# Kernel optimization log

Hardware: AMD Instinct MI355X
Metric: run time of the kernel (lower is better)

Reference implementation:

```python
import jax, jax.numpy as jnp
import numpy as np

N_HEAD = 16
BLOCK = 128  # segment length sl=128, dilation ratio dr=1 (hardcoded in forward)


def setup_inputs() -> dict:
    key = jax.random.key(0)
    k1, k2, k3 = jax.random.split(key, 3)
    B, T, C = 4, 8192, 2048
    x = jax.random.normal(k1, (B, T, C), dtype=jnp.float32)
    W_qkv = jax.random.normal(k2, (C, 3 * C), dtype=jnp.float32) * 0.02
    W_proj = jax.random.normal(k3, (C, C), dtype=jnp.float32) * 0.02
    return {"x": x, "W_qkv": W_qkv, "W_proj": W_proj}


def reference(x, W_qkv, W_proj):
    B, T, C = x.shape
    H = N_HEAD
    dh = C // H
    nb = T // BLOCK  # number of 128-token segments

    qkv = x @ W_qkv                      # (B, T, 3C)
    q, k, v = jnp.split(qkv, 3, axis=-1)

    def to_blocks(t):
        # (B, T, C) -> (B, nb, H, BLOCK, dh)
        return t.reshape(B, nb, BLOCK, H, dh).transpose(0, 1, 3, 2, 4)

    q, k, v = to_blocks(q), to_blocks(k), to_blocks(v)

    scale = 1.0 / jnp.sqrt(jnp.asarray(dh, dtype=x.dtype))
    scores = jnp.einsum('bnhqd,bnhkd->bnhqk', q, k) * scale  # (B, nb, H, BLOCK, BLOCK)
    causal = jnp.tril(jnp.ones((BLOCK, BLOCK), dtype=bool))
    scores = jnp.where(causal, scores, -jnp.inf)
    att = jax.nn.softmax(scores, axis=-1)
    out = jnp.einsum('bnhqk,bnhkd->bnhqd', att, v)
    # Single (sl, dr) branch => lse-weighted scattering collapses to weight 1.
    y = out.transpose(0, 1, 3, 2, 4).reshape(B, T, C)
    return y @ W_proj
```

## Files before the change

### kernel.cpp

```cpp
#include <hip/hip_runtime.h>

typedef unsigned short u16;
typedef unsigned int u32;
typedef __bf16 bf16x8 __attribute__((ext_vector_type(8)));
typedef float f32x4 __attribute__((ext_vector_type(4)));

#define DIM_M 32768
#define DIM_C 2048
#define DIM_3C 6144
#define N_HEAD 16
#define DH 128

__device__ __forceinline__ u16 f2bf(float f) {
  u32 x = __float_as_uint(f);
  u32 r = x + 0x7fffu + ((x >> 16) & 1u);
  return (u16)(r >> 16);
}

__device__ __forceinline__ void async_copy16(const void* g, void* l) {
  __builtin_amdgcn_global_load_lds((const __attribute__((address_space(1))) u32*)g,
                                   (__attribute__((address_space(3))) u32*)l,
                                   16, 0, 0);
}

__device__ __forceinline__ void phase_bar() {
  asm volatile("" ::: "memory");
  __builtin_amdgcn_sched_barrier(0);
  __builtin_amdgcn_s_barrier();
  __builtin_amdgcn_sched_barrier(0);
  asm volatile("" ::: "memory");
}

__global__ __launch_bounds__(256) void cvt_f32_bf16(const float* __restrict__ in,
                                                    u16* __restrict__ out) {
  size_t i = ((size_t)blockIdx.x * 256 + threadIdx.x) * 4;
  float4 v = *(const float4*)(in + i);
  union { u16 s[4]; uint2 u; } o;
  o.s[0] = f2bf(v.x); o.s[1] = f2bf(v.y); o.s[2] = f2bf(v.z); o.s[3] = f2bf(v.w);
  *(uint2*)(out + i) = o.u;
}

__global__ __launch_bounds__(256) void transpose_cvt(const float* __restrict__ W,
                                                     u16* __restrict__ Wt,
                                                     int K, int N) {
  __shared__ u16 t[32][33];
  int nb = blockIdx.x * 32, kb = blockIdx.y * 32;
  int r = threadIdx.x >> 5, c = threadIdx.x & 31;
#pragma unroll
  for (int i = 0; i < 4; ++i) {
    int rr = i * 8 + r;
    t[rr][c] = f2bf(W[(size_t)(kb + rr) * N + nb + c]);
  }
  __syncthreads();
#pragma unroll
  for (int i = 0; i < 4; ++i) {
    int rr = i * 8 + r;
    Wt[(size_t)(nb + rr) * K + kb + c] = t[c][rr];
  }
}

#define STAGE(OP, BUF, KOFF)                                                        \
  do {                                                                              \
    _Pragma("unroll") for (int l_ = 0; l_ < 4; ++l_)                                \
        async_copy16(g##OP + (size_t)l_ * 64 * K + (KOFF),                          \
                     &s##OP[BUF][(l_ * 8 + w) * 512]);                              \
  } while (0)

#define LDA_Q(QA)                                                                   \
  do {                                                                              \
    _Pragma("unroll") for (int f_ = 0; f_ < 4; ++f_)                                \
        _Pragma("unroll") for (int ks_ = 0; ks_ < 2; ++ks_) {                       \
      int r_ = WR + (QA) * 64 + f_ * 16 + ln15;                                     \
      a[f_][ks_] = *(const bf16x8*)&sAc[r_ * 64 + (((ks_ * 4 + quad) ^ (r_ & 7)) * 8)]; \
    }                                                                               \
  } while (0)

#define LDB_Q(QB)                                                                   \
  do {                                                                              \
    _Pragma("unroll") for (int f_ = 0; f_ < 2; ++f_)                                \
        _Pragma("unroll") for (int ks_ = 0; ks_ < 2; ++ks_) {                       \
      int r_ = WC + (QB) * 32 + f_ * 16 + ln15;                                     \
      b[f_][ks_] = *(const bf16x8*)&sBc[r_ * 64 + (((ks_ * 4 + quad) ^ (r_ & 7)) * 8)]; \
    }                                                                               \
  } while (0)

#define MMA_Q(QA, QB)                                                               \
  do {                                                                              \
    __builtin_amdgcn_s_setprio(1);                                                  \
    _Pragma("unroll") for (int ks_ = 0; ks_ < 2; ++ks_)                             \
        _Pragma("unroll") for (int f_ = 0; f_ < 4; ++f_)                            \
            _Pragma("unroll") for (int g_ = 0; g_ < 2; ++g_)                        \
                acc[(QA) * 4 + f_][(QB) * 2 + g_] =                                 \
        __builtin_amdgcn_mfma_f32_16x16x32_bf16(                                    \
            a[f_][ks_], b[g_][ks_], acc[(QA) * 4 + f_][(QB) * 2 + g_], 0, 0, 0);    \
    __builtin_amdgcn_s_setprio(0);                                                  \
  } while (0)

template <bool OUT_BF16>
__global__ __launch_bounds__(512, 2) void gemm256(const u16* __restrict__ A,
                                                  const u16* __restrict__ Bt,
                                                  void* __restrict__ Cv,
                                                  int M, int N, int K) {
  __shared__ u16 sA[2][256 * 64];
  __shared__ u16 sB[2][256 * 64];

  const int NT = N >> 8;
  int wg = blockIdx.x;
  {
    const int cpx = gridDim.x >> 3;
    wg = (wg & 7) * cpx + (wg >> 3);
  }
  const int rowblk = (wg / NT) << 8;
  const int colblk = (wg % NT) << 8;

  const int tid = threadIdx.x;
  const int w = tid >> 6, lane = tid & 63;
  const int ln15 = lane & 15, quad = lane >> 4;
  const int WR = (w >> 2) << 7;
  const int WC = (w & 3) << 6;

  const int srow = (w << 3) + (lane >> 3);
  const int scl = (lane & 7) ^ ((lane >> 3) & 7);
  const u16* gA = A + (size_t)(rowblk + srow) * K + scl * 8;
  const u16* gB = Bt + (size_t)(colblk + srow) * K + scl * 8;

  f32x4 acc[8][4] = {};
  bf16x8 a[4][2], b[2][2];
  const int KT = K >> 6;

  STAGE(A, 0, 0);
  STAGE(B, 0, 0);
  __syncthreads();

  for (int kt = 0; kt < KT; ++kt) {
    const int cur = kt & 1, nxt = cur ^ 1;
    const u16* sAc = sA[cur];
    const u16* sBc = sB[cur];
    const size_t gk = (size_t)(kt + 1) * 64;
    const bool pf = (kt + 1) < KT;

    if (pf) STAGE(A, nxt, gk);
    LDA_Q(0);
    LDB_Q(0);
    phase_bar();
    MMA_Q(0, 0);
    phase_bar();
    if (pf) STAGE(B, nxt, gk);
    LDB_Q(1);
    phase_bar();
    MMA_Q(0, 1);
    phase_bar();
    LDA_Q(1);
    phase_bar();
    MMA_Q(1, 1);
    phase_bar();
    LDB_Q(0);
    phase_bar();
    MMA_Q(1, 0);
    __syncthreads();
  }

#pragma unroll
  for (int fi = 0; fi < 8; ++fi) {
#pragma unroll
    for (int fj = 0; fj < 4; ++fj) {
      const float* ap = (const float*)&acc[fi][fj];
#pragma unroll
      for (int r = 0; r < 4; ++r) {
        int row = rowblk + WR + fi * 16 + quad * 4 + r;
        int col = colblk + WC + fj * 16 + ln15;
        if (OUT_BF16)
          ((u16*)Cv)[(size_t)row * N + col] = f2bf(ap[r]);
        else
          ((float*)Cv)[(size_t)row * N + col] = ap[r];
      }
    }
  }
}

__global__ __launch_bounds__(256) void attn_block(const u16* __restrict__ qkv,
                                                  u16* __restrict__ y) {
  __shared__ u16 buf0[128 * 128];
  __shared__ u16 buf1[128 * 128];
  const int h = blockIdx.x, n = blockIdx.y, b = blockIdx.z;
  const size_t rowbase = ((size_t)b * 8192 + (size_t)n * 128) * DIM_3C;
  const int qcol = h * DH, kcol = DIM_C + h * DH, vcol = 2 * DIM_C + h * DH;
  const int tid = threadIdx.x;
  const int wave = tid >> 6, lane = tid & 63;
  const int ln15 = lane & 15, quad = lane >> 4;
  const int r0 = wave * 32;

#pragma unroll
  for (int it = 0; it < 16; ++it) {
    int f = tid + it * 256;
    int tk = f >> 5;
    int dg = f & 31;
    int off = tk * 128 + (((dg >> 1) ^ (tk & 15)) * 8) + (dg & 1) * 4;
    uint2 qv = *(const uint2*)(qkv + rowbase + (size_t)tk * DIM_3C + qcol + dg * 4);
    *(uint2*)(buf0 + off) = qv;
    uint2 kv = *(const uint2*)(qkv + rowbase + (size_t)tk * DIM_3C + kcol + dg * 4);
    *(uint2*)(buf1 + off) = kv;
  }
  __syncthreads();

  f32x4 acc[2][8] = {};
#pragma unroll
  for (int ks = 0; ks < 4; ++ks) {
    bf16x8 aq[2], bk[8];
#pragma unroll
    for (int i = 0; i < 2; ++i) {
      int row = r0 + i * 16 + ln15;
      aq[i] = *(const bf16x8*)(buf0 + row * 128 + (((ks * 4 + quad) ^ (row & 15)) * 8));
    }
#pragma unroll
    for (int j = 0; j < 8; ++j) {
      int row = j * 16 + ln15;
      bk[j] = *(const bf16x8*)(buf1 + row * 128 + (((ks * 4 + quad) ^ (row & 15)) * 8));
    }
#pragma unroll
    for (int i = 0; i < 2; ++i)
#pragma unroll
      for (int j = 0; j < 8; ++j)
        acc[i][j] = __builtin_amdgcn_mfma_f32_16x16x32_bf16(aq[i], bk[j], acc[i][j], 0, 0, 0);
  }

  const float scale = 0.08838834764831845f;
  float lrow[2][4];
#pragma unroll
  for (int i = 0; i < 2; ++i) {
#pragma unroll
    for (int r = 0; r < 4; ++r) {
      int row = r0 + i * 16 + quad * 4 + r;
      float m = -1e30f;
#pragma unroll
      for (int j = 0; j < 8; ++j) {
        float* ap = (float*)&acc[i][j];
        int col = j * 16 + ln15;
        float s = ap[r] * scale;
        if (col > row) s = -1e30f;
        ap[r] = s;
        m = fmaxf(m, s);
      }
#pragma unroll
      for (int off = 1; off < 16; off <<= 1) m = fmaxf(m, __shfl_xor(m, off));
      float l = 0.f;
#pragma unroll
      for (int j = 0; j < 8; ++j) {
        float* ap = (float*)&acc[i][j];
        float p = __expf(ap[r] - m);
        ap[r] = p;
        l += p;
      }
#pragma unroll
      for (int off = 1; off < 16; off <<= 1) l += __shfl_xor(l, off);
      lrow[i][r] = l;
    }
  }
  __syncthreads();

#pragma unroll
  for (int i = 0; i < 2; ++i)
#pragma unroll
    for (int j = 0; j < 8; ++j) {
      const float* ap = (const float*)&acc[i][j];
#pragma unroll
      for (int r = 0; r < 4; ++r) {
        int row = r0 + i * 16 + quad * 4 + r;
        int col = j * 16 + ln15;
        buf0[row * 128 + (((col >> 3) ^ (row & 15)) * 8) + (col & 7)] = f2bf(ap[r]);
      }
    }
#pragma unroll
  for (int it = 0; it < 16; ++it) {
    int f = tid + it * 256;
    int tk = f >> 5;
    int dg = f & 31;
    uint2 vv = *(const uint2*)(qkv + rowbase + (size_t)tk * DIM_3C + vcol + dg * 4);
    union { u16 s[4]; uint2 u; } tmp;
    tmp.u = vv;
#pragma unroll
    for (int j = 0; j < 4; ++j) {
      int dd = dg * 4 + j;
      buf1[dd * 128 + (((tk >> 3) ^ (dd & 15)) * 8) + (tk & 7)] = tmp.s[j];
    }
  }
  __syncthreads();

  f32x4 accO[2][8] = {};
#pragma unroll
  for (int ks = 0; ks < 4; ++ks) {
    bf16x8 ap[2], bv[8];
#pragma unroll
    for (int i = 0; i < 2; ++i) {
      int row = r0 + i * 16 + ln15;
      ap[i] = *(const bf16x8*)(buf0 + row * 128 + (((ks * 4 + quad) ^ (row & 15)) * 8));
    }
#pragma unroll
    for (int j = 0; j < 8; ++j) {
      int row = j * 16 + ln15;
      bv[j] = *(const bf16x8*)(buf1 + row * 128 + (((ks * 4 + quad) ^ (row & 15)) * 8));
    }
#pragma unroll
    for (int i = 0; i < 2; ++i)
#pragma unroll
      for (int j = 0; j < 8; ++j)
        accO[i][j] = __builtin_amdgcn_mfma_f32_16x16x32_bf16(ap[i], bv[j], accO[i][j], 0, 0, 0);
  }

  u16* yb = y + ((size_t)b * 8192 + (size_t)n * 128) * DIM_C + h * DH;
#pragma unroll
  for (int i = 0; i < 2; ++i)
#pragma unroll
    for (int j = 0; j < 8; ++j) {
      const float* op = (const float*)&accO[i][j];
#pragma unroll
      for (int r = 0; r < 4; ++r) {
        int row = r0 + i * 16 + quad * 4 + r;
        int col = j * 16 + ln15;
        yb[(size_t)row * DIM_C + col] = f2bf(op[r] / lrow[i][r]);
      }
    }
}

extern "C" void kernel_launch(void* const* d_in, const int* in_sizes, int n_in,
                              void* d_out, int out_size, void* d_ws, size_t ws_size,
                              hipStream_t stream) {
  const float* x = (const float*)d_in[0];
  const float* W_qkv = (const float*)d_in[1];
  const float* W_proj = (const float*)d_in[2];
  float* out = (float*)d_out;

  char* ws = (char*)d_ws;
  u16* xb = (u16*)ws;
  u16* yb = xb;
  u16* qkvb = (u16*)(ws + (size_t)134217728);
  u16* Wqt = (u16*)(ws + (size_t)134217728 + 402653184);
  u16* Wpt = Wqt + (size_t)6144 * 2048;

  cvt_f32_bf16<<<dim3(65536), dim3(256), 0, stream>>>(x, xb);
  transpose_cvt<<<dim3(DIM_3C / 32, DIM_C / 32), dim3(256), 0, stream>>>(W_qkv, Wqt, DIM_C, DIM_3C);
  transpose_cvt<<<dim3(DIM_C / 32, DIM_C / 32), dim3(256), 0, stream>>>(W_proj, Wpt, DIM_C, DIM_C);
  gemm256<true><<<dim3((DIM_M / 256) * (DIM_3C / 256)), dim3(512), 0, stream>>>(
      xb, Wqt, (void*)qkvb, DIM_M, DIM_3C, DIM_C);
  attn_block<<<dim3(N_HEAD, 64, 4), dim3(256), 0, stream>>>(qkvb, yb);
  gemm256<false><<<dim3((DIM_M / 256) * (DIM_C / 256)), dim3(512), 0, stream>>>(
      yb, Wpt, (void*)out, DIM_M, DIM_C, DIM_C);
}
```

Before: 2.066 ms.

## Deepen GEMM pipeline to 4-stage BK=32 ring with explicit vmcnt waits

```diff
diff --git a/kernel.cpp b/kernel.cpp
--- a/kernel.cpp
+++ b/kernel.cpp
@@ -59,41 +59,11 @@
   }
 }
 
-#define STAGE(OP, BUF, KOFF)                                                        \
-  do {                                                                              \
-    _Pragma("unroll") for (int l_ = 0; l_ < 4; ++l_)                                \
-        async_copy16(g##OP + (size_t)l_ * 64 * K + (KOFF),                          \
-                     &s##OP[BUF][(l_ * 8 + w) * 512]);                              \
-  } while (0)
-
-#define LDA_Q(QA)                                                                   \
-  do {                                                                              \
-    _Pragma("unroll") for (int f_ = 0; f_ < 4; ++f_)                                \
-        _Pragma("unroll") for (int ks_ = 0; ks_ < 2; ++ks_) {                       \
-      int r_ = WR + (QA) * 64 + f_ * 16 + ln15;                                     \
-      a[f_][ks_] = *(const bf16x8*)&sAc[r_ * 64 + (((ks_ * 4 + quad) ^ (r_ & 7)) * 8)]; \
-    }                                                                               \
-  } while (0)
-
-#define LDB_Q(QB)                                                                   \
-  do {                                                                              \
-    _Pragma("unroll") for (int f_ = 0; f_ < 2; ++f_)                                \
-        _Pragma("unroll") for (int ks_ = 0; ks_ < 2; ++ks_) {                       \
-      int r_ = WC + (QB) * 32 + f_ * 16 + ln15;                                     \
-      b[f_][ks_] = *(const bf16x8*)&sBc[r_ * 64 + (((ks_ * 4 + quad) ^ (r_ & 7)) * 8)]; \
-    }                                                                               \
-  } while (0)
-
-#define MMA_Q(QA, QB)                                                               \
-  do {                                                                              \
-    __builtin_amdgcn_s_setprio(1);                                                  \
-    _Pragma("unroll") for (int ks_ = 0; ks_ < 2; ++ks_)                             \
-        _Pragma("unroll") for (int f_ = 0; f_ < 4; ++f_)                            \
-            _Pragma("unroll") for (int g_ = 0; g_ < 2; ++g_)                        \
-                acc[(QA) * 4 + f_][(QB) * 2 + g_] =                                 \
-        __builtin_amdgcn_mfma_f32_16x16x32_bf16(                                    \
-            a[f_][ks_], b[g_][ks_], acc[(QA) * 4 + f_][(QB) * 2 + g_], 0, 0, 0);    \
-    __builtin_amdgcn_s_setprio(0);                                                  \
+#define STAGE(OP, BUF, TT)                                                   \
+  do {                                                                       \
+    _Pragma("unroll") for (int l_ = 0; l_ < 2; ++l_)                         \
+        async_copy16(g##OP + (size_t)l_ * 128 * K + (size_t)(TT) * 32,       \
+                     &s##OP[BUF][(l_ * 128 + w * 16) * 32]);                 \
   } while (0)
 
 template <bool OUT_BF16>
@@ -101,8 +71,8 @@
                                                   const u16* __restrict__ Bt,
                                                   void* __restrict__ Cv,
                                                   int M, int N, int K) {
-  __shared__ u16 sA[2][256 * 64];
-  __shared__ u16 sB[2][256 * 64];
+  __shared__ u16 sA[4][256 * 32];
+  __shared__ u16 sB[4][256 * 32];
 
   const int NT = N >> 8;
   int wg = blockIdx.x;
@@ -119,45 +89,69 @@
   const int WR = (w >> 2) << 7;
   const int WC = (w & 3) << 6;
 
-  const int srow = (w << 3) + (lane >> 3);
-  const int scl = (lane & 7) ^ ((lane >> 3) & 7);
-  const u16* gA = A + (size_t)(rowblk + srow) * K + scl * 8;
-  const u16* gB = Bt + (size_t)(colblk + srow) * K + scl * 8;
+  const int srow = w * 16 + (lane >> 2);
+  const int schunk = (lane & 3) * 8;
+  const u16* gA = A + (size_t)(rowblk + srow) * K + schunk;
+  const u16* gB = Bt + (size_t)(colblk + srow) * K + schunk;
 
   f32x4 acc[8][4] = {};
-  bf16x8 a[4][2], b[2][2];
-  const int KT = K >> 6;
-
-  STAGE(A, 0, 0);
-  STAGE(B, 0, 0);
-  __syncthreads();
-
-  for (int kt = 0; kt < KT; ++kt) {
-    const int cur = kt & 1, nxt = cur ^ 1;
+  const int KT = K >> 5;
+
+#pragma unroll
+  for (int pt = 0; pt < 3; ++pt) {
+    STAGE(A, pt, pt);
+    STAGE(B, pt, pt);
+  }
+
+  for (int t = 0; t < KT; ++t) {
+    const int cur = t & 3;
     const u16* sAc = sA[cur];
     const u16* sBc = sB[cur];
-    const size_t gk = (size_t)(kt + 1) * 64;
-    const bool pf = (kt + 1) < KT;
-
-    if (pf) STAGE(A, nxt, gk);
-    LDA_Q(0);
-    LDB_Q(0);
+
+    if (t <= KT - 3)      asm volatile("s_waitcnt vmcnt(8)" ::: "memory");
+    else if (t == KT - 2) asm volatile("s_waitcnt vmcnt(4)" ::: "memory");
+    else                  asm volatile("s_waitcnt vmcnt(0)" ::: "memory");
     phase_bar();
-    MMA_Q(0, 0);
+
+    if (t + 3 < KT) {
+      STAGE(A, (t + 3) & 3, t + 3);
+      STAGE(B, (t + 3) & 3, t + 3);
+    }
+
+    bf16x8 a[4], b[4];
+#pragma unroll
+    for (int g = 0; g < 4; ++g) {
+      int r = WC + g * 16 + ln15;
+      b[g] = *(const bf16x8*)&sBc[r * 32 + quad * 8];
+    }
+#pragma unroll
+    for (int f = 0; f < 4; ++f) {
+      int r = WR + f * 16 + ln15;
+      a[f] = *(const bf16x8*)&sAc[r * 32 + quad * 8];
+    }
     phase_bar();
-    if (pf) STAGE(B, nxt, gk);
-    LDB_Q(1);
+    __builtin_amdgcn_s_setprio(1);
+#pragma unroll
+    for (int f = 0; f < 4; ++f)
+#pragma unroll
+      for (int g = 0; g < 4; ++g)
+        acc[f][g] = __builtin_amdgcn_mfma_f32_16x16x32_bf16(a[f], b[g], acc[f][g], 0, 0, 0);
+    __builtin_amdgcn_s_setprio(0);
+
+    bf16x8 a2[4];
+#pragma unroll
+    for (int f = 0; f < 4; ++f) {
+      int r = WR + 64 + f * 16 + ln15;
+      a2[f] = *(const bf16x8*)&sAc[r * 32 + quad * 8];
+    }
     phase_bar();
-    MMA_Q(0, 1);
-    phase_bar();
-    LDA_Q(1);
-    phase_bar();
-    MMA_Q(1, 1);
-    phase_bar();
-    LDB_Q(0);
-    phase_bar();
-    MMA_Q(1, 0);
-    __syncthreads();
+    __builtin_amdgcn_s_setprio(1);
+#pragma unroll
+    for (int f = 0; f < 4; ++f)
+#pragma unroll
+      for (int g = 0; g < 4; ++g)
+        acc[4 + f][g] = __builtin_amdgcn_mfma_f32_16x16x32_bf16(a2[f], b[g], acc[4 + f][g], 0, 0, 0);
+    __builtin_amdgcn_s_setprio(0);
   }
 
 #pragma unroll
```

After: 2.060 ms. About the same (-0.3%).
